# Performance work log

Measured on AMD Instinct MI355X. Metric: run time of the kernel, lower is better.

Reference implementation:

```python
import jax, jax.numpy as jnp
import numpy as np

TOTAL_QUBITS = 20  # state dim = 2**20
BATCH = 32


def setup_inputs() -> dict:
    key = jax.random.key(0)
    k1, k2 = jax.random.split(key)
    state = jax.random.normal(k1, (BATCH, 2 ** TOTAL_QUBITS), dtype=jnp.float32)
    theta = jax.random.normal(k2, (1,), dtype=jnp.float32)  # learned gate parameter
    qubit = 3  # static qubit index the gate acts on
    return {"state": state, "theta": theta, "qubit": qubit}


def _ry_matrix(theta):
    # RY(theta) = [[cos(t/2), -sin(t/2)], [sin(t/2), cos(t/2)]] -- purely real
    t = theta[0] / 2.0
    c, s = jnp.cos(t), jnp.sin(t)
    return jnp.stack([jnp.stack([c, -s]), jnp.stack([s, c])])  # [2, 2]


def reference(state, theta, qubit):
    B, dim = state.shape
    n = dim.bit_length() - 1  # total_qubits, static
    mat = _ry_matrix(theta)
    # view state as [B, 2, 2, ..., 2]; swap target qubit axis to front (matching
    # the torch permute which swaps positions 0 and qubit)
    x = state.reshape((B,) + (2,) * n)
    x = jnp.swapaxes(x, 1, 1 + qubit)
    x = x.reshape(B, 2, -1)                      # [B, gate_dim, rest]
    x = jnp.einsum('ij,bjk->bik', mat, x)        # tiny matmul over gate axis
    x = x.reshape((B,) + (2,) * n)
    x = jnp.swapaxes(x, 1, 1 + qubit)            # inverse permute
    return x.reshape(B, dim)
```

## Files before the change

kernel.cpp:

```cpp
#include <hip/hip_runtime.h>


typedef float floatx4 __attribute__((ext_vector_type(4)));

__global__ __launch_bounds__(256) void ry_gate_kernel(
    const float* __restrict__ in,
    const float* __restrict__ theta,
    const int*   __restrict__ qubit,
    float*       __restrict__ out,
    unsigned int n_waves)
{
    const unsigned int tid  = blockIdx.x * blockDim.x + threadIdx.x;
    const unsigned int wv   = tid >> 6;
    const unsigned int lane = threadIdx.x & 63u;
    if (wv >= n_waves) return;

    const int shift = 19 - qubit[0];
    const unsigned int stride = 1u << shift;
    const unsigned int mask   = stride - 1u;

    float t = theta[0] * 0.5f;
    float s, c;
    sincosf(t, &s, &c);

    const unsigned int e0 = wv * 512u + lane * 4u;
    const unsigned int i0 = (e0 & mask) | ((e0 & ~mask) << 1);
    const unsigned int j0 = i0 + 256u;
    const unsigned int i1 = i0 + stride;
    const unsigned int j1 = j0 + stride;

    floatx4 a0 = __builtin_nontemporal_load(reinterpret_cast<const floatx4*>(in + i0));
    floatx4 a1 = __builtin_nontemporal_load(reinterpret_cast<const floatx4*>(in + j0));
    floatx4 b0 = __builtin_nontemporal_load(reinterpret_cast<const floatx4*>(in + i1));
    floatx4 b1 = __builtin_nontemporal_load(reinterpret_cast<const floatx4*>(in + j1));

    floatx4 y00 = c * a0 - s * b0;
    floatx4 y01 = c * a1 - s * b1;
    floatx4 y10 = s * a0 + c * b0;
    floatx4 y11 = s * a1 + c * b1;

    __builtin_nontemporal_store(y00, reinterpret_cast<floatx4*>(out + i0));
    __builtin_nontemporal_store(y01, reinterpret_cast<floatx4*>(out + j0));
    __builtin_nontemporal_store(y10, reinterpret_cast<floatx4*>(out + i1));
    __builtin_nontemporal_store(y11, reinterpret_cast<floatx4*>(out + j1));
}

__global__ __launch_bounds__(256) void ry_gate_kernel_scalar(
    const float* __restrict__ in,
    const float* __restrict__ theta,
    const int*   __restrict__ qubit,
    float*       __restrict__ out,
    unsigned int n_pairs)
{
    unsigned int p = blockIdx.x * blockDim.x + threadIdx.x;
    if (p >= n_pairs) return;

    const int shift = 19 - qubit[0];
    const unsigned int stride = 1u << shift;
    const unsigned int mask   = stride - 1u;

    float t = theta[0] * 0.5f;
    float s, c;
    sincosf(t, &s, &c);

    unsigned int i0 = (p & mask) | ((p & ~mask) << 1);
    unsigned int i1 = i0 + stride;

    float x0 = in[i0], x1 = in[i1];
    out[i0] = c * x0 - s * x1;
    out[i1] = s * x0 + c * x1;
}

extern "C" void kernel_launch(void* const* d_in, const int* in_sizes, int n_in,
                              void* d_out, int out_size, void* d_ws, size_t ws_size,
                              hipStream_t stream)
{
    const float* state = (const float*)d_in[0];
    const float* theta = (const float*)d_in[1];
    const int*   qubit = (const int*)d_in[2];
    float*       out   = (float*)d_out;

    const unsigned int n_total = (unsigned int)in_sizes[0];
    const unsigned int n_waves = n_total / 1024u;
    const unsigned int n_thr   = n_waves * 64u;
    const int block = 256;
    const unsigned int grid = (n_thr + block - 1) / block;
    ry_gate_kernel<<<grid, block, 0, stream>>>(state, theta, qubit, out, n_waves);
}
```

Before: 225.1 us.

## Use persistent grid-stride loop with software-prefetched next chunk loads

Caps the grid at 2048 blocks and turns the kernel into a grid-stride loop. Each wave loads the next chunk's four vectors before computing and storing the current one, so memory loads overlap with stores. This reduces block launch overhead, at the cost of fewer waves in flight per CU and higher register use for the prefetched data.

```diff
diff --git a/kernel.cpp b/kernel.cpp
--- a/kernel.cpp
+++ b/kernel.cpp
@@ -8,12 +8,13 @@
     const float* __restrict__ theta,
     const int*   __restrict__ qubit,
     float*       __restrict__ out,
-    unsigned int n_waves)
+    unsigned int n_chunks)
 {
+    const unsigned int n_act_waves = (gridDim.x * blockDim.x) >> 6;
     const unsigned int tid  = blockIdx.x * blockDim.x + threadIdx.x;
-    const unsigned int wv   = tid >> 6;
     const unsigned int lane = threadIdx.x & 63u;
-    if (wv >= n_waves) return;
+    unsigned int chunk = tid >> 6;
+    if (chunk >= n_chunks) return;
 
     const int shift = 19 - qubit[0];
     const unsigned int stride = 1u << shift;
@@ -23,26 +24,52 @@
     float s, c;
     sincosf(t, &s, &c);
 
-    const unsigned int e0 = wv * 512u + lane * 4u;
-    const unsigned int i0 = (e0 & mask) | ((e0 & ~mask) << 1);
-    const unsigned int j0 = i0 + 256u;
-    const unsigned int i1 = i0 + stride;
-    const unsigned int j1 = j0 + stride;
+    const unsigned int loff = lane * 4u;
+
+    unsigned int e0 = chunk * 512u + loff;
+    unsigned int i0 = (e0 & mask) | ((e0 & ~mask) << 1);
+    unsigned int j0 = i0 + 256u;
+    unsigned int i1 = i0 + stride;
+    unsigned int j1 = j0 + stride;
 
     floatx4 a0 = __builtin_nontemporal_load(reinterpret_cast<const floatx4*>(in + i0));
     floatx4 a1 = __builtin_nontemporal_load(reinterpret_cast<const floatx4*>(in + j0));
     floatx4 b0 = __builtin_nontemporal_load(reinterpret_cast<const floatx4*>(in + i1));
     floatx4 b1 = __builtin_nontemporal_load(reinterpret_cast<const floatx4*>(in + j1));
 
-    floatx4 y00 = c * a0 - s * b0;
-    floatx4 y01 = c * a1 - s * b1;
-    floatx4 y10 = s * a0 + c * b0;
-    floatx4 y11 = s * a1 + c * b1;
+    for (;;) {
+        const unsigned int next = chunk + n_act_waves;
+        const bool have_next = next < n_chunks;
 
-    __builtin_nontemporal_store(y00, reinterpret_cast<floatx4*>(out + i0));
-    __builtin_nontemporal_store(y01, reinterpret_cast<floatx4*>(out + j0));
-    __builtin_nontemporal_store(y10, reinterpret_cast<floatx4*>(out + i1));
-    __builtin_nontemporal_store(y11, reinterpret_cast<floatx4*>(out + j1));
+        unsigned int ni0 = 0, nj0 = 0, ni1 = 0, nj1 = 0;
+        floatx4 na0, na1, nb0, nb1;
+        if (have_next) {
+            unsigned int ne = next * 512u + loff;
+            ni0 = (ne & mask) | ((ne & ~mask) << 1);
+            nj0 = ni0 + 256u;
+            ni1 = ni0 + stride;
+            nj1 = nj0 + stride;
+            na0 = __builtin_nontemporal_load(reinterpret_cast<const floatx4*>(in + ni0));
+            na1 = __builtin_nontemporal_load(reinterpret_cast<const floatx4*>(in + nj0));
+            nb0 = __builtin_nontemporal_load(reinterpret_cast<const floatx4*>(in + ni1));
+            nb1 = __builtin_nontemporal_load(reinterpret_cast<const floatx4*>(in + nj1));
+        }
+
+        floatx4 y00 = c * a0 - s * b0;
+        floatx4 y01 = c * a1 - s * b1;
+        floatx4 y10 = s * a0 + c * b0;
+        floatx4 y11 = s * a1 + c * b1;
+
+        __builtin_nontemporal_store(y00, reinterpret_cast<floatx4*>(out + i0));
+        __builtin_nontemporal_store(y01, reinterpret_cast<floatx4*>(out + j0));
+        __builtin_nontemporal_store(y10, reinterpret_cast<floatx4*>(out + i1));
+        __builtin_nontemporal_store(y11, reinterpret_cast<floatx4*>(out + j1));
+
+        if (!have_next) break;
+        chunk = next;
+        i0 = ni0; j0 = nj0; i1 = ni1; j1 = nj1;
+        a0 = na0; a1 = na1; b0 = nb0; b1 = nb1;
+    }
 }
 
 __global__ __launch_bounds__(256) void ry_gate_kernel_scalar(
@@ -80,10 +107,10 @@
     const int*   qubit = (const int*)d_in[2];
     float*       out   = (float*)d_out;
 
-    const unsigned int n_total = (unsigned int)in_sizes[0];
-    const unsigned int n_waves = n_total / 1024u;
-    const unsigned int n_thr   = n_waves * 64u;
+    const unsigned int n_total  = (unsigned int)in_sizes[0];
+    const unsigned int n_chunks = n_total / 1024u;
     const int block = 256;
-    const unsigned int grid = (n_thr + block - 1) / block;
-    ry_gate_kernel<<<grid, block, 0, stream>>>(state, theta, qubit, out, n_waves);
+    unsigned int grid = (n_chunks * 64u + block - 1) / block;
+    if (grid > 2048u) grid = 2048u;
+    ry_gate_kernel<<<grid, block, 0, stream>>>(state, theta, qubit, out, n_chunks);
 }
```

New measurement: 225.1 us. About the same (-0.0%).
